# Kernel optimization log

Measured on AMD Instinct MI355X. Metric: run time of the kernel, lower is better.

The kernel has to match this reference:

```python
import jax, jax.numpy as jnp
import numpy as np

B = 65536      # batch size
XD = 64        # x_dim: number of DAG nodes / tabular features
HD = 128       # h_dim
F_SCALE = 0.1  # f_scale weight shrink applied after xavier init


def _xavier(key, shape, fan_in, fan_out, scale):
    std = float(np.sqrt(2.0 / (fan_in + fan_out)))
    return jax.random.normal(key, shape, jnp.float32) * (std * scale)


def setup_inputs() -> dict:
    key = jax.random.key(0)
    ks = jax.random.split(key, 8)
    x = jax.random.uniform(ks[0], (B, XD), jnp.float32)
    z = jax.random.normal(ks[1], (B, XD, 1), jnp.float32)  # noise regenerated inside torch forward
    # learnable soft adjacency M: rand*0.2 with zero diagonal (dag_seed == [])
    M = jax.random.uniform(ks[2], (XD, XD), jnp.float32) * 0.2
    M = M * (1.0 - jnp.eye(XD, dtype=jnp.float32))
    # per-node input layers fc_i[i]: Linear(XD+1, HD), xavier*f_scale, column i zeroed (1e-16)
    Wi = _xavier(ks[3], (XD, HD, XD + 1), XD + 1, HD, F_SCALE)
    idx = jnp.arange(XD)
    Wi = Wi.at[idx, :, idx].set(1e-16)
    bi = jnp.zeros((XD, HD), jnp.float32)
    # shared MLP: Linear(HD,HD)+ReLU twice, xavier*f_scale
    Ws1 = _xavier(ks[4], (HD, HD), HD, HD, F_SCALE)
    bs1 = jnp.zeros((HD,), jnp.float32)
    Ws2 = _xavier(ks[5], (HD, HD), HD, HD, F_SCALE)
    bs2 = jnp.zeros((HD,), jnp.float32)
    # per-node output heads fc_f[i]: Linear(HD, 1), xavier*f_scale
    wf = _xavier(ks[6], (XD, HD), HD, 1, F_SCALE)
    bf = jnp.zeros((XD,), jnp.float32)
    return {"x": x, "z": z, "M": M, "Wi": Wi, "bi": bi, "Ws1": Ws1,
            "bs1": bs1, "Ws2": Ws2, "bs2": bs2, "wf": wf, "bf": bf}


def reference(x, z, M, Wi, bi, Ws1, bs1, Ws2, bs2, wf, bf):
    # Generator_causal.sequential with choice='original', gen_order=range(XD), biased_edges={}
    zT = jnp.transpose(z, (1, 0, 2))  # [XD, B, 1], z[:, i, :] per step
    Mcols = M.T                       # row i == M[:, i] (parent mask of node i)
    idx = jnp.arange(XD)

    def step(out, xs):
        i, mcol, Wi_i, bi_i, wf_i, bf_i, z_i = xs
        xm = out * mcol                         # adjacency-masked parent gather [B, XD]
        xm = xm.at[:, i].set(0.0)               # x_masked[:, i] = 0
        h = jnp.concatenate([xm, z_i], axis=1)  # [B, XD+1]
        h = jax.nn.relu(h @ Wi_i.T + bi_i)      # fc_i[i] + ReLU
        h = jax.nn.relu(h @ Ws1.T + bs1)        # shared block 1
        h = jax.nn.relu(h @ Ws2.T + bs2)        # shared block 2
        o = jax.nn.sigmoid(h @ wf_i + bf_i)     # fc_f[i] -> [B]
        out = out.at[:, i].set(o)               # scatter write into out[:, i]
        return out, None

    out, _ = jax.lax.scan(step, x, (idx, Mcols, Wi, bi, wf, bf, zT))
    return out
```

## Files before the change

### kernel.cpp

```cpp
#include <hip/hip_runtime.h>

#define XD 64
#define HD 128
#define RB 128
#define NT 512
#define BLOB 18432
#define N_STEP_CHUNKS 18

#define OFF_STEP0 0
#define OFF_STEP1 18432
#define OFF_H1    36864
#define OFF_H2    69632
#define OFF_WS2   102400
#define OFF_OUT   135168
#define OFF_ZC    151552
#define OFF_BS1   152576
#define OFF_BS2   153088
#define SMEM_BYTES 153600

typedef __attribute__((ext_vector_type(8))) short short8;
typedef __attribute__((ext_vector_type(4))) float f32x4;
typedef unsigned int u32;

__device__ __forceinline__ short f2bf(float f) {
    union { float f; unsigned u; } v; v.f = f;
    unsigned r = (v.u + 0x7FFFu + ((v.u >> 16) & 1u)) >> 16;
    return (short)r;
}
__device__ __forceinline__ float bf2f(short s) {
    union { float f; unsigned u; } v;
    v.u = ((unsigned)(unsigned short)s) << 16;
    return v.f;
}

__device__ __forceinline__ void* swz128(char* base, int row, int byteoff) {
    return base + row * 128 + (byteoff ^ ((row & 7) << 4));
}
__device__ __forceinline__ void* swz256(char* base, int row, int byteoff) {
    return base + row * 256 + (byteoff ^ ((row & 7) << 4));
}

__device__ __forceinline__ void gload16(const void* g, void* l) {
    __builtin_amdgcn_global_load_lds(
        (const __attribute__((address_space(1))) u32*)g,
        (__attribute__((address_space(3))) u32*)l, 16, 0, 0);
}

__global__ void prep_kernel(const float* __restrict__ Wi, const float* __restrict__ M,
                            const float* __restrict__ bi, const float* __restrict__ wf,
                            const float* __restrict__ bf, char* __restrict__ ws)
{
    int idx = blockIdx.x * 256 + threadIdx.x;
    if (idx < XD * HD * 8) {
        int i  = idx >> 10;
        int n  = (idx >> 3) & 127;
        int kc = idx & 7;
        const float* src = Wi + ((size_t)i * HD + n) * (XD + 1) + kc * 8;
        short8 v;
        #pragma unroll
        for (int j = 0; j < 8; ++j) {
            int k = kc * 8 + j;
            float m = (k == i) ? 0.0f : M[k * XD + i];
            v[j] = f2bf(src[j] * m);
        }
        char* dst = ws + (size_t)i * BLOB + n * 128 + ((kc * 16) ^ ((n & 7) << 4));
        *(short8*)dst = v;
    } else {
        int r = idx - XD * HD * 8;
        if (r < XD * HD) {
            int i = r >> 7, n = r & 127;
            float* d = (float*)(ws + (size_t)i * BLOB + 16384);
            d[n]       = Wi[((size_t)i * HD + n) * (XD + 1) + XD];
            d[128 + n] = bi[i * HD + n];
            d[256 + n] = wf[i * HD + n];
            if (n == 0) d[384] = bf[i];
        }
    }
}

__global__ __launch_bounds__(NT, 1) void gen_kernel(
    const float* __restrict__ x,   const float* __restrict__ z,
    const float* __restrict__ Ws1, const float* __restrict__ Ws2,
    const float* __restrict__ bs1, const float* __restrict__ bs2,
    const char*  __restrict__ blob, float* __restrict__ out)
{
    extern __shared__ char smem[];
    const int tid  = threadIdx.x;
    const int row0 = blockIdx.x * RB;
    const int wave = tid >> 6, lane = tid & 63;
    const int lg = lane >> 4, lc = lane & 15;
    const int wm = wave >> 2, wn = wave & 3;

    char*  sH1  = smem + OFF_H1;
    char*  sH2  = smem + OFF_H2;
    char*  sWS2 = smem + OFF_WS2;
    char*  sOUT = smem + OFF_OUT;
    float* sBS1 = (float*)(smem + OFF_BS1);
    float* sBS2 = (float*)(smem + OFF_BS2);

    for (int c = wave; c < N_STEP_CHUNKS; c += 8)
        gload16(blob + c * 1024 + lane * 16, smem + OFF_STEP0 + c * 1024);
    if (tid < RB)
        ((float*)(smem + OFF_ZC))[tid] = z[(size_t)(row0 + tid) * XD + 0];
    for (int c = tid; c < RB * 8; c += NT) {
        int r = c >> 3, kc = c & 7;
        const float* xs = x + (size_t)(row0 + r) * XD + kc * 8;
        short8 v;
        #pragma unroll
        for (int j = 0; j < 8; ++j) v[j] = f2bf(xs[j]);
        *(short8*)swz128(sOUT, r, kc * 16) = v;
    }
    for (int c = tid; c < HD * 16; c += NT) {
        int n = c >> 4, kc = c & 15;
        const float* wsrc = Ws2 + n * HD + kc * 8;
        short8 v;
        #pragma unroll
        for (int j = 0; j < 8; ++j) v[j] = f2bf(wsrc[j]);
        *(short8*)swz256(sWS2, n, kc * 16) = v;
    }
    if (tid < HD) { sBS1[tid] = bs1[tid]; sBS2[tid] = bs2[tid]; }

    short8 BW1[2][4];
    #pragma unroll
    for (int t = 0; t < 2; ++t) {
        int n = wn * 32 + t * 16 + lc;
        #pragma unroll
        for (int s = 0; s < 4; ++s) {
            const float* p = Ws1 + n * HD + s * 32 + lg * 8;
            #pragma unroll
            for (int j = 0; j < 8; ++j) BW1[t][s][j] = f2bf(p[j]);
        }
    }
    __syncthreads();

    float zreg = 0.f;
    for (int i = 0; i < XD; ++i) {
        char* sWIb = smem + ((i & 1) ? OFF_STEP1 : OFF_STEP0);
        char* sWIn = smem + ((i & 1) ? OFF_STEP0 : OFF_STEP1);
        const float* blobS = (const float*)(sWIb + 16384);
        float* zcur = (float*)(smem + OFF_ZC) + (i & 1) * 128;
        float* znxt = (float*)(smem + OFF_ZC) + ((i + 1) & 1) * 128;

        if (i + 1 < XD) {
            const char* gb = blob + (size_t)(i + 1) * BLOB;
            for (int c = wave; c < N_STEP_CHUNKS; c += 8)
                gload16(gb + c * 1024 + lane * 16, sWIn + c * 1024);
            if (tid < RB) zreg = z[(size_t)(row0 + tid) * XD + (i + 1)];
        }

        short8 a0[4], a1[4], b0[2], b1[2];
        #pragma unroll
        for (int m = 0; m < 4; ++m) {
            int row = wm * 64 + m * 16 + lc;
            a0[m] = *(const short8*)swz128(sOUT, row, lg * 16);
            a1[m] = *(const short8*)swz128(sOUT, row, 64 + lg * 16);
        }
        #pragma unroll
        for (int t = 0; t < 2; ++t) {
            int n = wn * 32 + t * 16 + lc;
            b0[t] = *(const short8*)swz128(sWIb, n, lg * 16);
            b1[t] = *(const short8*)swz128(sWIb, n, 64 + lg * 16);
        }
        float zrow[4][4];
        #pragma unroll
        for (int m = 0; m < 4; ++m) {
            f32x4 zv = *(const f32x4*)&zcur[wm * 64 + m * 16 + lg * 4];
            #pragma unroll
            for (int j = 0; j < 4; ++j) zrow[m][j] = zv[j];
        }
        #pragma unroll
        for (int t = 0; t < 2; ++t) {
            int n = wn * 32 + t * 16 + lc;
            float wizn = blobS[n], bin = blobS[128 + n];
            #pragma unroll
            for (int m = 0; m < 4; ++m) {
                f32x4 c = {0.f, 0.f, 0.f, 0.f};
                c = __builtin_amdgcn_mfma_f32_16x16x32_bf16(a0[m], b0[t], c, 0, 0, 0);
                c = __builtin_amdgcn_mfma_f32_16x16x32_bf16(a1[m], b1[t], c, 0, 0, 0);
                #pragma unroll
                for (int j = 0; j < 4; ++j) {
                    int row = wm * 64 + m * 16 + lg * 4 + j;
                    float v = c[j] + zrow[m][j] * wizn + bin;
                    *(short*)swz256(sH1, row, 2 * n) = f2bf(fmaxf(v, 0.f));
                }
            }
        }
        __syncthreads();

        #pragma unroll
        for (int m = 0; m < 4; ++m) {
            int row = wm * 64 + m * 16 + lc;
            short8 A2[4];
            #pragma unroll
            for (int s = 0; s < 4; ++s)
                A2[s] = *(const short8*)swz256(sH1, row, s * 64 + lg * 16);
            #pragma unroll
            for (int t = 0; t < 2; ++t) {
                f32x4 c = {0.f, 0.f, 0.f, 0.f};
                #pragma unroll
                for (int s = 0; s < 4; ++s)
                    c = __builtin_amdgcn_mfma_f32_16x16x32_bf16(A2[s], BW1[t][s], c, 0, 0, 0);
                int n = wn * 32 + t * 16 + lc;
                float bn = sBS1[n];
                #pragma unroll
                for (int j = 0; j < 4; ++j) {
                    int wrow = wm * 64 + m * 16 + lg * 4 + j;
                    *(short*)swz256(sH2, wrow, 2 * n) = f2bf(fmaxf(c[j] + bn, 0.f));
                }
            }
        }
        __syncthreads();

        {
            int mrow = wave * 16 + lc;
            short8 A3[4];
            #pragma unroll
            for (int s = 0; s < 4; ++s)
                A3[s] = *(const short8*)swz256(sH2, mrow, s * 64 + lg * 16);
            float op[4] = {0.f, 0.f, 0.f, 0.f};
            #pragma unroll
            for (int tp = 0; tp < 8; ++tp) {
                int n = tp * 16 + lc;
                f32x4 c = {0.f, 0.f, 0.f, 0.f};
                #pragma unroll
                for (int s = 0; s < 4; ++s) {
                    short8 b = *(const short8*)swz256(sWS2, n, s * 64 + lg * 16);
                    c = __builtin_amdgcn_mfma_f32_16x16x32_bf16(A3[s], b, c, 0, 0, 0);
                }
                float bn = sBS2[n], wfn = blobS[256 + n];
                #pragma unroll
                for (int j = 0; j < 4; ++j)
                    op[j] += fmaxf(c[j] + bn, 0.f) * wfn;
            }
            #pragma unroll
            for (int msk = 1; msk < 16; msk <<= 1) {
                #pragma unroll
                for (int j = 0; j < 4; ++j)
                    op[j] += __shfl_xor(op[j], msk, 64);
            }
            if (i + 1 < XD && tid < RB) znxt[tid] = zreg;
            if (lc < 4) {
                float o = op[lc] + blobS[384];
                o = 1.0f / (1.0f + __expf(-o));
                int row = wave * 16 + lg * 4 + lc;
                *(short*)swz128(sOUT, row, 2 * i) = f2bf(o);
            }
        }
        __syncthreads();
    }

    for (int c = tid; c < RB * 8; c += NT) {
        int r = c >> 3, kc = c & 7;
        short8 v = *(const short8*)swz128(sOUT, r, kc * 16);
        float* o = out + (size_t)(row0 + r) * XD + kc * 8;
        #pragma unroll
        for (int j = 0; j < 8; ++j) o[j] = bf2f(v[j]);
    }
}

extern "C" void kernel_launch(void* const* d_in, const int* in_sizes, int n_in,
                              void* d_out, int out_size, void* d_ws, size_t ws_size,
                              hipStream_t stream) {
    const float* x   = (const float*)d_in[0];
    const float* z   = (const float*)d_in[1];
    const float* M   = (const float*)d_in[2];
    const float* Wi  = (const float*)d_in[3];
    const float* bi  = (const float*)d_in[4];
    const float* Ws1 = (const float*)d_in[5];
    const float* bs1 = (const float*)d_in[6];
    const float* Ws2 = (const float*)d_in[7];
    const float* bs2 = (const float*)d_in[8];
    const float* wf  = (const float*)d_in[9];
    const float* bf  = (const float*)d_in[10];
    float* outp = (float*)d_out;
    char*  ws   = (char*)d_ws;

    prep_kernel<<<288, 256, 0, stream>>>(Wi, M, bi, wf, bf, ws);

    hipFuncSetAttribute(reinterpret_cast<const void*>(gen_kernel),
                        hipFuncAttributeMaxDynamicSharedMemorySize, SMEM_BYTES);
    gen_kernel<<<65536 / RB, NT, SMEM_BYTES, stream>>>(
        x, z, Ws1, Ws2, bs1, bs2, ws, outp);
}
```

Measured before the change: 663.9 us.

## Transpose MFMA operands, hold Ws2 in registers, pack hidden-state stores

Swaps the A and B operands of every MFMA so the accumulator runs along hidden units, not batch rows. This lets bias initialise the accumulator and lets each lane store four bf16 hidden values in one 8-byte LDS write instead of scalar 2-byte writes. Ws2 now lives in registers (BW2) instead of LDS, which removes its per-step LDS reads and shrinks shared memory enough that launch bounds can request two blocks per CU. The final reduction over columns needs only two shuffles. The risk is register pressure: 128 VGPRs of BW2 plus BW1 under a two-block bound may cause spilling.

```diff
diff --git a/kernel.cpp b/kernel.cpp
--- a/kernel.cpp
+++ b/kernel.cpp
@@ -11,15 +11,15 @@
 #define OFF_STEP1 18432
 #define OFF_H1    36864
 #define OFF_H2    69632
-#define OFF_WS2   102400
-#define OFF_OUT   135168
-#define OFF_ZC    151552
-#define OFF_BS1   152576
-#define OFF_BS2   153088
-#define SMEM_BYTES 153600
+#define OFF_OUT   102400
+#define OFF_ZC    118784
+#define OFF_BS1   119808
+#define OFF_BS2   120320
+#define SMEM_BYTES 120832
 
 typedef __attribute__((ext_vector_type(8))) short short8;
 typedef __attribute__((ext_vector_type(4))) float f32x4;
+typedef __attribute__((ext_vector_type(2))) unsigned int u32x2;
 typedef unsigned int u32;
 
 __device__ __forceinline__ short f2bf(float f) {
@@ -31,6 +31,9 @@
     union { float f; unsigned u; } v;
     v.u = ((unsigned)(unsigned short)s) << 16;
     return v.f;
+}
+__device__ __forceinline__ u32 pack2(float a, float b) {
+    return (u32)(unsigned short)f2bf(a) | ((u32)(unsigned short)f2bf(b) << 16);
 }
 
 __device__ __forceinline__ void* swz128(char* base, int row, int byteoff) {
@@ -78,7 +81,7 @@
     }
 }
 
-__global__ __launch_bounds__(NT, 1) void gen_kernel(
+__global__ __launch_bounds__(NT, 2) void gen_kernel(
     const float* __restrict__ x,   const float* __restrict__ z,
     const float* __restrict__ Ws1, const float* __restrict__ Ws2,
     const float* __restrict__ bs1, const float* __restrict__ bs2,
@@ -93,15 +96,15 @@
 
     char*  sH1  = smem + OFF_H1;
     char*  sH2  = smem + OFF_H2;
-    char*  sWS2 = smem + OFF_WS2;
     char*  sOUT = smem + OFF_OUT;
+    float* sZC  = (float*)(smem + OFF_ZC);
     float* sBS1 = (float*)(smem + OFF_BS1);
     float* sBS2 = (float*)(smem + OFF_BS2);
 
     for (int c = wave; c < N_STEP_CHUNKS; c += 8)
         gload16(blob + c * 1024 + lane * 16, smem + OFF_STEP0 + c * 1024);
     if (tid < RB)
-        ((float*)(smem + OFF_ZC))[tid] = z[(size_t)(row0 + tid) * XD + 0];
+        sZC[tid] = z[(size_t)(row0 + tid) * XD + 0];
     for (int c = tid; c < RB * 8; c += NT) {
         int r = c >> 3, kc = c & 7;
         const float* xs = x + (size_t)(row0 + r) * XD + kc * 8;
@@ -110,14 +113,6 @@
         for (int j = 0; j < 8; ++j) v[j] = f2bf(xs[j]);
         *(short8*)swz128(sOUT, r, kc * 16) = v;
     }
-    for (int c = tid; c < HD * 16; c += NT) {
-        int n = c >> 4, kc = c & 15;
-        const float* wsrc = Ws2 + n * HD + kc * 8;
-        short8 v;
-        #pragma unroll
-        for (int j = 0; j < 8; ++j) v[j] = f2bf(wsrc[j]);
-        *(short8*)swz256(sWS2, n, kc * 16) = v;
-    }
     if (tid < HD) { sBS1[tid] = bs1[tid]; sBS2[tid] = bs2[tid]; }
 
     short8 BW1[2][4];
@@ -129,6 +124,17 @@
             const float* p = Ws1 + n * HD + s * 32 + lg * 8;
             #pragma unroll
             for (int j = 0; j < 8; ++j) BW1[t][s][j] = f2bf(p[j]);
+        }
+    }
+    short8 BW2[8][4];
+    #pragma unroll
+    for (int tp = 0; tp < 8; ++tp) {
+        int n = tp * 16 + lc;
+        #pragma unroll
+        for (int s = 0; s < 4; ++s) {
+            const float* p = Ws2 + n * HD + s * 32 + lg * 8;
+            #pragma unroll
+            for (int j = 0; j < 8; ++j) BW2[tp][s][j] = f2bf(p[j]);
         }
     }
     __syncthreads();
@@ -138,8 +144,8 @@
         char* sWIb = smem + ((i & 1) ? OFF_STEP1 : OFF_STEP0);
         char* sWIn = smem + ((i & 1) ? OFF_STEP0 : OFF_STEP1);
         const float* blobS = (const float*)(sWIb + 16384);
-        float* zcur = (float*)(smem + OFF_ZC) + (i & 1) * 128;
-        float* znxt = (float*)(smem + OFF_ZC) + ((i + 1) & 1) * 128;
+        float* zcur = sZC + (i & 1) * 128;
+        float* znxt = sZC + ((i + 1) & 1) * 128;
 
         if (i + 1 < XD) {
             const char* gb = blob + (size_t)(i + 1) * BLOB;
@@ -148,102 +154,91 @@
             if (tid < RB) zreg = z[(size_t)(row0 + tid) * XD + (i + 1)];
         }
 
-        short8 a0[4], a1[4], b0[2], b1[2];
-        #pragma unroll
-        for (int m = 0; m < 4; ++m) {
-            int row = wm * 64 + m * 16 + lc;
-            a0[m] = *(const short8*)swz128(sOUT, row, lg * 16);
-            a1[m] = *(const short8*)swz128(sOUT, row, 64 + lg * 16);
-        }
+        short8 aW[2][2], bO[4][2];
         #pragma unroll
         for (int t = 0; t < 2; ++t) {
             int n = wn * 32 + t * 16 + lc;
-            b0[t] = *(const short8*)swz128(sWIb, n, lg * 16);
-            b1[t] = *(const short8*)swz128(sWIb, n, 64 + lg * 16);
-        }
-        float zrow[4][4];
+            aW[t][0] = *(const short8*)swz128(sWIb, n, lg * 16);
+            aW[t][1] = *(const short8*)swz128(sWIb, n, 64 + lg * 16);
+        }
         #pragma unroll
         for (int m = 0; m < 4; ++m) {
-            f32x4 zv = *(const f32x4*)&zcur[wm * 64 + m * 16 + lg * 4];
-            #pragma unroll
-            for (int j = 0; j < 4; ++j) zrow[m][j] = zv[j];
-        }
+            int r = wm * 64 + m * 16 + lc;
+            bO[m][0] = *(const short8*)swz128(sOUT, r, lg * 16);
+            bO[m][1] = *(const short8*)swz128(sOUT, r, 64 + lg * 16);
+        }
+        float zm[4];
+        #pragma unroll
+        for (int m = 0; m < 4; ++m) zm[m] = zcur[wm * 64 + m * 16 + lc];
+
         #pragma unroll
         for (int t = 0; t < 2; ++t) {
-            int n = wn * 32 + t * 16 + lc;
-            float wizn = blobS[n], bin = blobS[128 + n];
+            int nb = wn * 32 + t * 16;
+            f32x4 wiz = *(const f32x4*)&blobS[nb + lg * 4];
+            f32x4 bi4 = *(const f32x4*)&blobS[128 + nb + lg * 4];
             #pragma unroll
             for (int m = 0; m < 4; ++m) {
-                f32x4 c = {0.f, 0.f, 0.f, 0.f};
-                c = __builtin_amdgcn_mfma_f32_16x16x32_bf16(a0[m], b0[t], c, 0, 0, 0);
-                c = __builtin_amdgcn_mfma_f32_16x16x32_bf16(a1[m], b1[t], c, 0, 0, 0);
-                #pragma unroll
-                for (int j = 0; j < 4; ++j) {
-                    int row = wm * 64 + m * 16 + lg * 4 + j;
-                    float v = c[j] + zrow[m][j] * wizn + bin;
-                    *(short*)swz256(sH1, row, 2 * n) = f2bf(fmaxf(v, 0.f));
-                }
+                f32x4 c = bi4;
+                c = __builtin_amdgcn_mfma_f32_16x16x32_bf16(aW[t][0], bO[m][0], c, 0, 0, 0);
+                c = __builtin_amdgcn_mfma_f32_16x16x32_bf16(aW[t][1], bO[m][1], c, 0, 0, 0);
+                float v0 = fmaxf(c[0] + zm[m] * wiz[0], 0.f);
+                float v1 = fmaxf(c[1] + zm[m] * wiz[1], 0.f);
+                float v2 = fmaxf(c[2] + zm[m] * wiz[2], 0.f);
+                float v3 = fmaxf(c[3] + zm[m] * wiz[3], 0.f);
+                u32x2 w = { pack2(v0, v1), pack2(v2, v3) };
+                int r = wm * 64 + m * 16 + lc;
+                *(u32x2*)swz256(sH1, r, 2 * nb + lg * 8) = w;
             }
         }
         __syncthreads();
 
         #pragma unroll
         for (int m = 0; m < 4; ++m) {
-            int row = wm * 64 + m * 16 + lc;
-            short8 A2[4];
+            int r = wm * 64 + m * 16 + lc;
+            short8 bH[4];
             #pragma unroll
             for (int s = 0; s < 4; ++s)
-                A2[s] = *(const short8*)swz256(sH1, row, s * 64 + lg * 16);
+                bH[s] = *(const short8*)swz256(sH1, r, s * 64 + lg * 16);
             #pragma unroll
             for (int t = 0; t < 2; ++t) {
-                f32x4 c = {0.f, 0.f, 0.f, 0.f};
+                int nb = wn * 32 + t * 16;
+                f32x4 c = *(const f32x4*)&sBS1[nb + lg * 4];
                 #pragma unroll
                 for (int s = 0; s < 4; ++s)
-                    c = __builtin_amdgcn_mfma_f32_16x16x32_bf16(A2[s], BW1[t][s], c, 0, 0, 0);
-                int n = wn * 32 + t * 16 + lc;
-                float bn = sBS1[n];
+                    c = __builtin_amdgcn_mfma_f32_16x16x32_bf16(BW1[t][s], bH[s], c, 0, 0, 0);
+                u32x2 w = { pack2(fmaxf(c[0], 0.f), fmaxf(c[1], 0.f)),
+                            pack2(fmaxf(c[2], 0.f), fmaxf(c[3], 0.f)) };
+                *(u32x2*)swz256(sH2, r, 2 * nb + lg * 8) = w;
+            }
+        }
+        __syncthreads();
+
+        {
+            int r = wave * 16 + lc;
+            short8 bH[4];
+            #pragma unroll
+            for (int s = 0; s < 4; ++s)
+                bH[s] = *(const short8*)swz256(sH2, r, s * 64 + lg * 16);
+            float op = 0.f;
+            #pragma unroll
+            for (int tp = 0; tp < 8; ++tp) {
+                f32x4 c = *(const f32x4*)&sBS2[tp * 16 + lg * 4];
                 #pragma unroll
-                for (int j = 0; j < 4; ++j) {
-                    int wrow = wm * 64 + m * 16 + lg * 4 + j;
-                    *(short*)swz256(sH2, wrow, 2 * n) = f2bf(fmaxf(c[j] + bn, 0.f));
-                }
-            }
-        }
-        __syncthreads();
-
-        {
-            int mrow = wave * 16 + lc;
-            short8 A3[4];
-            #pragma unroll
-            for (int s = 0; s < 4; ++s)
-                A3[s] = *(const short8*)swz256(sH2, mrow, s * 64 + lg * 16);
-            float op[4] = {0.f, 0.f, 0.f, 0.f};
-            #pragma unroll
-            for (int tp = 0; tp < 8; ++tp) {
-                int n = tp * 16 + lc;
-                f32x4 c = {0.f, 0.f, 0.f, 0.f};
-                #pragma unroll
-                for (int s = 0; s < 4; ++s) {
-                    short8 b = *(const short8*)swz256(sWS2, n, s * 64 + lg * 16);
-                    c = __builtin_amdgcn_mfma_f32_16x16x32_bf16(A3[s], b, c, 0, 0, 0);
-                }
-                float bn = sBS2[n], wfn = blobS[256 + n];
-                #pragma unroll
-                for (int j = 0; j < 4; ++j)
-                    op[j] += fmaxf(c[j] + bn, 0.f) * wfn;
-            }
-            #pragma unroll
-            for (int msk = 1; msk < 16; msk <<= 1) {
-                #pragma unroll
-                for (int j = 0; j < 4; ++j)
-                    op[j] += __shfl_xor(op[j], msk, 64);
-            }
+                for (int s = 0; s < 4; ++s)
+                    c = __builtin_amdgcn_mfma_f32_16x16x32_bf16(BW2[tp][s], bH[s], c, 0, 0, 0);
+                f32x4 wf4 = *(const f32x4*)&blobS[256 + tp * 16 + lg * 4];
+                op += fmaxf(c[0], 0.f) * wf4[0];
+                op += fmaxf(c[1], 0.f) * wf4[1];
+                op += fmaxf(c[2], 0.f) * wf4[2];
+                op += fmaxf(c[3], 0.f) * wf4[3];
+            }
+            op += __shfl_xor(op, 16, 64);
+            op += __shfl_xor(op, 32, 64);
             if (i + 1 < XD && tid < RB) znxt[tid] = zreg;
-            if (lc < 4) {
-                float o = op[lc] + blobS[384];
+            if (lg == 0) {
+                float o = op + blobS[384];
                 o = 1.0f / (1.0f + __expf(-o));
-                int row = wave * 16 + lg * 4 + lc;
-                *(short*)swz128(sOUT, row, 2 * i) = f2bf(o);
+                *(short*)swz128(sOUT, r, 2 * i) = f2bf(o);
             }
         }
         __syncthreads();
```

Measured after the change: 699.7 us. 1.05x slower.
